# Optimization experiments

Hardware: AMD Instinct MI355X
Metric: run time of the kernel (lower is better)

## Reference

```python
import jax, jax.numpy as jnp
import numpy as np

DECAY_MIN = 0.9
DECAY_MAX = 0.999

def setup_inputs() -> dict:
    key = jax.random.key(0)
    ks = jax.random.split(key, 6)
    B, L, D, M = 8, 4096, 1024, 64
    s = 0.02
    return {
        "x": jax.random.normal(ks[0], (B, L, D), jnp.float32),
        "Wq": jax.random.normal(ks[1], (D, M), jnp.float32) * s,
        "Wk": jax.random.normal(ks[2], (D, M), jnp.float32) * s,
        "Wv": jax.random.normal(ks[3], (D, M), jnp.float32) * s,
        "Wo": jax.random.normal(ks[4], (M, D), jnp.float32) * s,
        "bo": jnp.zeros((D,), jnp.float32),
        "Wg": jax.random.normal(ks[5], (D, 1), jnp.float32) * s,
        "bg": jnp.zeros((1,), jnp.float32),
        "decay_param": jnp.full((1,), 0.5, jnp.float32),
    }

def reference(x, Wq, Wk, Wv, Wo, bo, Wg, bg, decay_param):
    B, L, D = x.shape
    M = Wq.shape[1]
    # decay in [DECAY_MIN, DECAY_MAX], shape (1,) -> scalar broadcast
    decay = DECAY_MIN + jax.nn.sigmoid(decay_param) * (DECAY_MAX - DECAY_MIN)
    q = x @ Wq  # (B,L,M)
    k = x @ Wk
    v = x @ Wv
    gates = jax.nn.sigmoid(x @ Wg + bg)[..., 0]  # (B,L)
    S0 = jnp.zeros((B, M, M), x.dtype)

    def scan_fn(S, inp):
        q_t, k_t, v_t, g_t = inp  # (B,M),(B,M),(B,M),(B,)
        gk = k_t * g_t[:, None]
        gv = v_t * g_t[:, None]
        # fast-weight update: S = decay*S + gk ⊗ gv
        S = decay * S + gk[:, :, None] * gv[:, None, :]
        out_t = jnp.einsum('bd,bde->be', q_t, S)
        return S, out_t

    S_final, outs = jax.lax.scan(
        scan_fn, S0,
        (q.transpose(1, 0, 2), k.transpose(1, 0, 2), v.transpose(1, 0, 2), gates.T))
    outs = outs.transpose(1, 0, 2)  # (B,L,M)
    y = outs @ Wo + bo  # (B,L,D); dropout deterministic (eval)
    return y, S_final
```

## Files before the change

kernel.cpp:

```cpp
#include <hip/hip_runtime.h>
#include <math.h>

#define B_SZ 8
#define L_SZ 4096
#define D_SZ 1024
#define M_SZ 64
#define ROWS (B_SZ * L_SZ)
#define NCHUNK 64
#define CHUNK 64

#define FMA4(acc, sc, v) { (acc).x += (sc)*(v).x; (acc).y += (sc)*(v).y; (acc).z += (sc)*(v).z; (acc).w += (sc)*(v).w; }
#define SCALE4(v, sc) { (v).x *= (sc); (v).y *= (sc); (v).z *= (sc); (v).w *= (sc); }

typedef __attribute__((ext_vector_type(8))) short bf16x8;
typedef __attribute__((ext_vector_type(4))) float f32x4;

__device__ __forceinline__ float sigmoid_f(float z) { return 1.0f / (1.0f + __expf(-z)); }
__device__ __forceinline__ float decay_of(const float* __restrict__ dp) {
  return 0.9f + (0.999f - 0.9f) * sigmoid_f(dp[0]);
}
__device__ __forceinline__ unsigned short f2bf(float f) {
  unsigned int u = __float_as_uint(f);
  unsigned int r = (u + 0x7FFFu + ((u >> 16) & 1u)) >> 16;
  return (unsigned short)r;
}

__global__ __launch_bounds__(256) void k0_prep(
    const float* __restrict__ Wq, const float* __restrict__ Wk,
    const float* __restrict__ Wv, unsigned short* __restrict__ Wt)
{
  const int n = blockIdx.x;
  const float* src = (n < 64) ? Wq : (n < 128) ? Wk : Wv;
  const int nc = n & 63;
  #pragma unroll
  for (int j = 0; j < 4; ++j) {
    int k = threadIdx.x + 256 * j;
    Wt[(size_t)n * D_SZ + k] = f2bf(src[(size_t)k * 64 + nc]);
  }
}

#define K1_ROWS 128
#define K1_LDA 72
#define K1_LDB 72

__global__ __launch_bounds__(256, 1) void k1_qkvg_mfma(
    const float* __restrict__ x, const unsigned short* __restrict__ Wt,
    const float* __restrict__ Wg, const float* __restrict__ bg,
    float* __restrict__ q_ws, float* __restrict__ a_ws, float* __restrict__ b_ws)
{
  __shared__ __align__(16) unsigned short As[K1_ROWS * K1_LDA];
  __shared__ __align__(16) unsigned short Bs[192 * K1_LDB];
  __shared__ float Wgs[64];
  __shared__ float Gs[K1_ROWS];

  const int tid  = threadIdx.x;
  const int lane = tid & 63;
  const int w    = tid >> 6;
  const int quad = lane >> 4;
  const int l15  = lane & 15;
  const int row0 = blockIdx.x * K1_ROWS;

  const int srow = tid >> 1;
  const int skh  = tid & 1;

  f32x4 acc[2][12];
  #pragma unroll
  for (int tr = 0; tr < 2; ++tr)
    #pragma unroll
    for (int tn = 0; tn < 12; ++tn)
      acc[tr][tn] = (f32x4){0.f, 0.f, 0.f, 0.f};

  float gacc = 0.f;

  for (int k0 = 0; k0 < D_SZ; k0 += 64) {
    float4 xa[8];
    const float* xp = x + (size_t)(row0 + srow) * D_SZ + k0 + skh * 32;
    #pragma unroll
    for (int j = 0; j < 8; ++j) xa[j] = *reinterpret_cast<const float4*>(xp + 4 * j);
    uint4 bb[6];
    #pragma unroll
    for (int i = 0; i < 6; ++i) {
      int cid = tid + 256 * i;
      int n = cid >> 3, c = cid & 7;
      bb[i] = *reinterpret_cast<const uint4*>(Wt + (size_t)n * D_SZ + k0 + 8 * c);
    }
    float4 wgv = make_float4(0, 0, 0, 0);
    if (tid < 16) wgv = *reinterpret_cast<const float4*>(Wg + k0 + 4 * tid);

    __syncthreads();

    #pragma unroll
    for (int j = 0; j < 4; ++j) {
      uint4 p;
      p.x = (unsigned)f2bf(xa[2*j].x)   | ((unsigned)f2bf(xa[2*j].y)   << 16);
      p.y = (unsigned)f2bf(xa[2*j].z)   | ((unsigned)f2bf(xa[2*j].w)   << 16);
      p.z = (unsigned)f2bf(xa[2*j+1].x) | ((unsigned)f2bf(xa[2*j+1].y) << 16);
      p.w = (unsigned)f2bf(xa[2*j+1].z) | ((unsigned)f2bf(xa[2*j+1].w) << 16);
      *reinterpret_cast<uint4*>(&As[srow * K1_LDA + skh * 32 + 8 * j]) = p;
    }
    #pragma unroll
    for (int i = 0; i < 6; ++i) {
      int cid = tid + 256 * i;
      int n = cid >> 3, c = cid & 7;
      *reinterpret_cast<uint4*>(&Bs[n * K1_LDB + 8 * c]) = bb[i];
    }
    if (tid < 16) *reinterpret_cast<float4*>(&Wgs[4 * tid]) = wgv;
    __syncthreads();

    #pragma unroll
    for (int j = 0; j < 8; ++j) {
      float4 wv = *reinterpret_cast<float4*>(&Wgs[skh * 32 + 4 * j]);
      gacc += xa[j].x * wv.x + xa[j].y * wv.y + xa[j].z * wv.z + xa[j].w * wv.w;
    }

    #pragma unroll
    for (int kt = 0; kt < 2; ++kt) {
      bf16x8 af0 = *reinterpret_cast<bf16x8*>(&As[(32 * w +      l15) * K1_LDA + kt * 32 + quad * 8]);
      bf16x8 af1 = *reinterpret_cast<bf16x8*>(&As[(32 * w + 16 + l15) * K1_LDA + kt * 32 + quad * 8]);
      #pragma unroll
      for (int tn = 0; tn < 12; ++tn) {
        bf16x8 bfv = *reinterpret_cast<bf16x8*>(&Bs[(tn * 16 + l15) * K1_LDB + kt * 32 + quad * 8]);
        acc[0][tn] = __builtin_amdgcn_mfma_f32_16x16x32_bf16(af0, bfv, acc[0][tn], 0, 0, 0);
        acc[1][tn] = __builtin_amdgcn_mfma_f32_16x16x32_bf16(af1, bfv, acc[1][tn], 0, 0, 0);
      }
    }
  }

  float gfull = gacc + __shfl_xor(gacc, 1);
  if ((tid & 1) == 0) Gs[srow] = sigmoid_f(gfull + bg[0]);
  __syncthreads();

  #pragma unroll
  for (int tr = 0; tr < 2; ++tr) {
    const int rbase = 32 * w + 16 * tr + quad * 4;
    #pragma unroll
    for (int tn = 0; tn < 12; ++tn) {
      const int ncol = (tn & 3) * 16 + l15;
      float* dst = (tn < 4) ? q_ws : (tn < 8 ? a_ws : b_ws);
      #pragma unroll
      for (int r = 0; r < 4; ++r) {
        const int rl = rbase + r;
        float vv = acc[tr][tn][r];
        if (tn >= 4) vv *= Gs[rl];
        dst[(size_t)(row0 + rl) * 64 + ncol] = vv;
      }
    }
  }
}

__global__ __launch_bounds__(256) void k2_delta(
    const float* __restrict__ a_ws, const float* __restrict__ b_ws,
    const float* __restrict__ dp, float* __restrict__ dS)
{
  __shared__ float Aa[64][64];
  __shared__ float Bc[64][64];
  __shared__ float pw[64];
  const int tid = threadIdx.x;
  const int bc = blockIdx.x;
  const int rowbase = (bc >> 6) * L_SZ + (bc & 63) * CHUNK;
  const int s = tid >> 2, m0 = (tid & 3) * 16;
  #pragma unroll
  for (int j = 0; j < 4; ++j) {
    *reinterpret_cast<float4*>(&Aa[s][m0 + 4*j]) =
        *reinterpret_cast<const float4*>(&a_ws[(size_t)(rowbase + s) * 64 + m0 + 4*j]);
    *reinterpret_cast<float4*>(&Bc[s][m0 + 4*j]) =
        *reinterpret_cast<const float4*>(&b_ws[(size_t)(rowbase + s) * 64 + m0 + 4*j]);
  }
  if (tid < 64) pw[tid] = powf(decay_of(dp), (float)(63 - tid));
  __syncthreads();
  const int d0 = tid >> 2, e0 = (tid & 3) * 16;
  float4 o0 = make_float4(0,0,0,0), o1 = o0, o2 = o0, o3 = o0;
  for (int ss = 0; ss < 64; ++ss) {
    float wa = pw[ss] * Aa[ss][d0];
    float4 b0 = *reinterpret_cast<float4*>(&Bc[ss][e0+0]);
    float4 b1 = *reinterpret_cast<float4*>(&Bc[ss][e0+4]);
    float4 b2 = *reinterpret_cast<float4*>(&Bc[ss][e0+8]);
    float4 b3 = *reinterpret_cast<float4*>(&Bc[ss][e0+12]);
    FMA4(o0, wa, b0); FMA4(o1, wa, b1); FMA4(o2, wa, b2); FMA4(o3, wa, b3);
  }
  float* dst = &dS[((size_t)bc << 12) + d0 * 64 + e0];
  *reinterpret_cast<float4*>(dst + 0)  = o0;
  *reinterpret_cast<float4*>(dst + 4)  = o1;
  *reinterpret_cast<float4*>(dst + 8)  = o2;
  *reinterpret_cast<float4*>(dst + 12) = o3;
}

__global__ __launch_bounds__(256) void k3_scan(
    const float* __restrict__ dS, const float* __restrict__ dp,
    float* __restrict__ Sst, float* __restrict__ sfin)
{
  const int g = blockIdx.x * 256 + threadIdx.x;
  const int b = g >> 12;
  const int de = g & 4095;
  const float dC = powf(decay_of(dp), 64.0f);
  float s = 0.f;
  for (int c = 0; c < NCHUNK; ++c) {
    const size_t idx = ((size_t)(b * 64 + c) << 12) + de;
    Sst[idx] = s;
    s = dC * s + dS[idx];
  }
  sfin[((size_t)b << 12) + de] = s;
}

__global__ __launch_bounds__(256) void k4_intra(
    const float* __restrict__ q_ws, const float* __restrict__ a_ws,
    const float* __restrict__ b_ws, const float* __restrict__ Sst,
    const float* __restrict__ dp, float* __restrict__ outs)
{
  __shared__ float Qs[64][68];
  __shared__ float Ps[64][68];
  __shared__ float Bs[64][64];
  __shared__ float S0s[64][64];
  __shared__ float pw[65];
  const int tid = threadIdx.x;
  const int bc = blockIdx.x;
  const int rowbase = (bc >> 6) * L_SZ + (bc & 63) * CHUNK;
  const int s = tid >> 2, m0 = (tid & 3) * 16;
  #pragma unroll
  for (int j = 0; j < 4; ++j) {
    float4 qv = *reinterpret_cast<const float4*>(&q_ws[(size_t)(rowbase + s) * 64 + m0 + 4*j]);
    Qs[s][m0+4*j+0] = qv.x; Qs[s][m0+4*j+1] = qv.y; Qs[s][m0+4*j+2] = qv.z; Qs[s][m0+4*j+3] = qv.w;
    float4 av = *reinterpret_cast<const float4*>(&a_ws[(size_t)(rowbase + s) * 64 + m0 + 4*j]);
    Ps[m0+4*j+0][s] = av.x; Ps[m0+4*j+1][s] = av.y; Ps[m0+4*j+2][s] = av.z; Ps[m0+4*j+3][s] = av.w;
    float4 bv = *reinterpret_cast<const float4*>(&b_ws[(size_t)(rowbase + s) * 64 + m0 + 4*j]);
    *reinterpret_cast<float4*>(&Bs[s][m0+4*j]) = bv;
    float4 sv = *reinterpret_cast<const float4*>(&Sst[((size_t)bc << 12) + tid*16 + 4*j]);
    *reinterpret_cast<float4*>(&(&S0s[0][0])[tid*16 + 4*j]) = sv;
  }
  if (tid < 65) pw[tid] = powf(decay_of(dp), (float)tid);
  __syncthreads();

  const int t0 = tid >> 2, c0 = (tid & 3) * 16;
  float4 r0 = make_float4(0,0,0,0), r1 = r0, r2 = r0, r3 = r0;
  for (int m = 0; m < 64; ++m) {
    float qv = Qs[t0][m];
    float4 a0 = *reinterpret_cast<float4*>(&Ps[m][c0+0]);
    float4 a1 = *reinterpret_cast<float4*>(&Ps[m][c0+4]);
    float4 a2 = *reinterpret_cast<float4*>(&Ps[m][c0+8]);
    float4 a3 = *reinterpret_cast<float4*>(&Ps[m][c0+12]);
    FMA4(r0, qv, a0); FMA4(r1, qv, a1); FMA4(r2, qv, a2); FMA4(r3, qv, a3);
  }
  float rr[16] = {r0.x,r0.y,r0.z,r0.w, r1.x,r1.y,r1.z,r1.w,
                  r2.x,r2.y,r2.z,r2.w, r3.x,r3.y,r3.z,r3.w};
  __syncthreads();
  #pragma unroll
  for (int j = 0; j < 16; ++j) {
    const int sidx = c0 + j;
    Ps[t0][sidx] = (sidx <= t0) ? rr[j] * pw[t0 - sidx] : 0.f;
  }
  __syncthreads();

  float4 o0 = make_float4(0,0,0,0), o1 = o0, o2 = o0, o3 = o0;
  for (int m = 0; m < 64; ++m) {
    float qv = Qs[t0][m];
    float4 v0 = *reinterpret_cast<float4*>(&S0s[m][c0+0]);
    float4 v1 = *reinterpret_cast<float4*>(&S0s[m][c0+4]);
    float4 v2 = *reinterpret_cast<float4*>(&S0s[m][c0+8]);
    float4 v3 = *reinterpret_cast<float4*>(&S0s[m][c0+12]);
    FMA4(o0, qv, v0); FMA4(o1, qv, v1); FMA4(o2, qv, v2); FMA4(o3, qv, v3);
  }
  const float dsc = pw[t0 + 1];
  SCALE4(o0, dsc); SCALE4(o1, dsc); SCALE4(o2, dsc); SCALE4(o3, dsc);
  for (int ss = 0; ss < 64; ++ss) {
    float pv = Ps[t0][ss];
    float4 b0 = *reinterpret_cast<float4*>(&Bs[ss][c0+0]);
    float4 b1 = *reinterpret_cast<float4*>(&Bs[ss][c0+4]);
    float4 b2 = *reinterpret_cast<float4*>(&Bs[ss][c0+8]);
    float4 b3 = *reinterpret_cast<float4*>(&Bs[ss][c0+12]);
    FMA4(o0, pv, b0); FMA4(o1, pv, b1); FMA4(o2, pv, b2); FMA4(o3, pv, b3);
  }
  float* dst = &outs[(size_t)(rowbase + t0) * 64 + c0];
  *reinterpret_cast<float4*>(dst + 0)  = o0;
  *reinterpret_cast<float4*>(dst + 4)  = o1;
  *reinterpret_cast<float4*>(dst + 8)  = o2;
  *reinterpret_cast<float4*>(dst + 12) = o3;
}

__global__ __launch_bounds__(256) void k5_proj(
    const float* __restrict__ outs, const float* __restrict__ Wo,
    const float* __restrict__ bo, float* __restrict__ y)
{
  __shared__ float Os[64][68];
  __shared__ float Ws[64][64];
  const int tid = threadIdx.x;
  const int tx = tid & 15, ty = tid >> 4;
  const int row0 = blockIdx.x * 64;
  const int n0 = blockIdx.y * 64;
  const int s = tid >> 2, m0 = (tid & 3) * 16;
  #pragma unroll
  for (int j = 0; j < 4; ++j) {
    float4 ov = *reinterpret_cast<const float4*>(&outs[(size_t)(row0 + s) * 64 + m0 + 4*j]);
    Os[s][m0+4*j+0] = ov.x; Os[s][m0+4*j+1] = ov.y; Os[s][m0+4*j+2] = ov.z; Os[s][m0+4*j+3] = ov.w;
    float4 wv = *reinterpret_cast<const float4*>(&Wo[(size_t)s * D_SZ + n0 + m0 + 4*j]);
    *reinterpret_cast<float4*>(&Ws[s][m0+4*j]) = wv;
  }
  __syncthreads();
  float4 acc[4];
  #pragma unroll
  for (int r = 0; r < 4; ++r) acc[r] = make_float4(0,0,0,0);
  for (int kk = 0; kk < 64; ++kk) {
    float a0 = Os[4*ty+0][kk];
    float a1 = Os[4*ty+1][kk];
    float a2 = Os[4*ty+2][kk];
    float a3 = Os[4*ty+3][kk];
    float4 w = *reinterpret_cast<float4*>(&Ws[kk][4*tx]);
    FMA4(acc[0], a0, w); FMA4(acc[1], a1, w); FMA4(acc[2], a2, w); FMA4(acc[3], a3, w);
  }
  float4 bv = *reinterpret_cast<const float4*>(&bo[n0 + 4*tx]);
  #pragma unroll
  for (int r = 0; r < 4; ++r) {
    float4 res;
    res.x = acc[r].x + bv.x; res.y = acc[r].y + bv.y;
    res.z = acc[r].z + bv.z; res.w = acc[r].w + bv.w;
    *reinterpret_cast<float4*>(&y[(size_t)(row0 + 4*ty + r) * D_SZ + n0 + 4*tx]) = res;
  }
}

extern "C" void kernel_launch(void* const* d_in, const int* in_sizes, int n_in,
                              void* d_out, int out_size, void* d_ws, size_t ws_size,
                              hipStream_t stream) {
  (void)in_sizes; (void)n_in; (void)out_size; (void)ws_size;
  const float* x  = (const float*)d_in[0];
  const float* Wq = (const float*)d_in[1];
  const float* Wk = (const float*)d_in[2];
  const float* Wv = (const float*)d_in[3];
  const float* Wo = (const float*)d_in[4];
  const float* bo = (const float*)d_in[5];
  const float* Wg = (const float*)d_in[6];
  const float* bg = (const float*)d_in[7];
  const float* dp = (const float*)d_in[8];

  float* y    = (float*)d_out;
  float* sfin = y + (size_t)B_SZ * L_SZ * D_SZ;

  float* ws   = (float*)d_ws;
  const size_t SEG = (size_t)ROWS * M_SZ;
  float* q_ws = ws;
  float* a_ws = q_ws + SEG;
  float* b_ws = a_ws + SEG;
  float* dS   = b_ws + SEG;
  float* Sst  = dS   + SEG;
  float* outs = Sst  + SEG;
  unsigned short* Wt = (unsigned short*)outs;

  k0_prep<<<dim3(192), dim3(256), 0, stream>>>(Wq, Wk, Wv, Wt);
  k1_qkvg_mfma<<<dim3(ROWS / K1_ROWS), dim3(256), 0, stream>>>(x, Wt, Wg, bg, q_ws, a_ws, b_ws);
  k2_delta<<<dim3(B_SZ * NCHUNK), dim3(256), 0, stream>>>(a_ws, b_ws, dp, dS);
  k3_scan<<<dim3((B_SZ * M_SZ * M_SZ) / 256), dim3(256), 0, stream>>>(dS, dp, Sst, sfin);
  k4_intra<<<dim3(B_SZ * NCHUNK), dim3(256), 0, stream>>>(q_ws, a_ws, b_ws, Sst, dp, outs);
  k5_proj<<<dim3(ROWS / 64, D_SZ / 64), dim3(256), 0, stream>>>(outs, Wo, bo, y);
}
```

Measured before the change: 385.6 us.

## Double-buffer QKV GEMM with direct register A-fragments, smaller tiles; batch scan loads

The projection kernel now uses 64-row tiles at two blocks per CU. Each wave loads its x rows from global memory straight into MFMA A-fragments in registers, skipping the LDS staging for A. The weight tile is double-buffered in LDS with the next tile's loads issued before the current MFMAs, so one barrier per iteration remains. The gate is reduced by lane shuffles instead of shared memory. The chunk scan kernel also loads all 64 chunk deltas into registers up front to expose memory-level parallelism. The costs are higher register pressure and B tiles that are now re-read from L2 by twice as many blocks.

```diff
diff --git a/kernel.cpp b/kernel.cpp
--- a/kernel.cpp
+++ b/kernel.cpp
@@ -39,19 +39,16 @@
   }
 }
 
-#define K1_ROWS 128
-#define K1_LDA 72
+#define K1_ROWS 64
 #define K1_LDB 72
 
-__global__ __launch_bounds__(256, 1) void k1_qkvg_mfma(
+__global__ __launch_bounds__(256, 2) void k1_qkvg_mfma(
     const float* __restrict__ x, const unsigned short* __restrict__ Wt,
     const float* __restrict__ Wg, const float* __restrict__ bg,
     float* __restrict__ q_ws, float* __restrict__ a_ws, float* __restrict__ b_ws)
 {
-  __shared__ __align__(16) unsigned short As[K1_ROWS * K1_LDA];
-  __shared__ __align__(16) unsigned short Bs[192 * K1_LDB];
-  __shared__ float Wgs[64];
-  __shared__ float Gs[K1_ROWS];
+  __shared__ __align__(16) unsigned short Bs[2][192 * K1_LDB];
+  __shared__ float Wgs[D_SZ];
 
   const int tid  = threadIdx.x;
   const int lane = tid & 63;
@@ -60,90 +57,101 @@
   const int l15  = lane & 15;
   const int row0 = blockIdx.x * K1_ROWS;
 
-  const int srow = tid >> 1;
-  const int skh  = tid & 1;
-
-  f32x4 acc[2][12];
-  #pragma unroll
-  for (int tr = 0; tr < 2; ++tr)
-    #pragma unroll
-    for (int tn = 0; tn < 12; ++tn)
-      acc[tr][tn] = (f32x4){0.f, 0.f, 0.f, 0.f};
-
-  float gacc = 0.f;
-
-  for (int k0 = 0; k0 < D_SZ; k0 += 64) {
-    float4 xa[8];
-    const float* xp = x + (size_t)(row0 + srow) * D_SZ + k0 + skh * 32;
-    #pragma unroll
-    for (int j = 0; j < 8; ++j) xa[j] = *reinterpret_cast<const float4*>(xp + 4 * j);
-    uint4 bb[6];
+  const float* xrow = x + (size_t)(row0 + 16 * w + l15) * D_SZ;
+
+  f32x4 acc[12];
+  #pragma unroll
+  for (int tn = 0; tn < 12; ++tn) acc[tn] = (f32x4){0.f, 0.f, 0.f, 0.f};
+
+  uint4  bb[6];
+  float4 xa[4];
+  bf16x8 af[2];
+  float  gacc = 0.f;
+
+  *reinterpret_cast<float4*>(&Wgs[4 * tid]) = *reinterpret_cast<const float4*>(Wg + 4 * tid);
+
+  auto loadB = [&](int k0) {
     #pragma unroll
     for (int i = 0; i < 6; ++i) {
       int cid = tid + 256 * i;
       int n = cid >> 3, c = cid & 7;
       bb[i] = *reinterpret_cast<const uint4*>(Wt + (size_t)n * D_SZ + k0 + 8 * c);
     }
-    float4 wgv = make_float4(0, 0, 0, 0);
-    if (tid < 16) wgv = *reinterpret_cast<const float4*>(Wg + k0 + 4 * tid);
-
-    __syncthreads();
-
-    #pragma unroll
-    for (int j = 0; j < 4; ++j) {
-      uint4 p;
-      p.x = (unsigned)f2bf(xa[2*j].x)   | ((unsigned)f2bf(xa[2*j].y)   << 16);
-      p.y = (unsigned)f2bf(xa[2*j].z)   | ((unsigned)f2bf(xa[2*j].w)   << 16);
-      p.z = (unsigned)f2bf(xa[2*j+1].x) | ((unsigned)f2bf(xa[2*j+1].y) << 16);
-      p.w = (unsigned)f2bf(xa[2*j+1].z) | ((unsigned)f2bf(xa[2*j+1].w) << 16);
-      *reinterpret_cast<uint4*>(&As[srow * K1_LDA + skh * 32 + 8 * j]) = p;
-    }
+  };
+  auto loadA = [&](int k0) {
+    #pragma unroll
+    for (int kt = 0; kt < 2; ++kt)
+      #pragma unroll
+      for (int j = 0; j < 2; ++j)
+        xa[kt * 2 + j] = *reinterpret_cast<const float4*>(xrow + k0 + kt * 32 + quad * 8 + 4 * j);
+  };
+  auto writeB = [&](int buf) {
     #pragma unroll
     for (int i = 0; i < 6; ++i) {
       int cid = tid + 256 * i;
       int n = cid >> 3, c = cid & 7;
-      *reinterpret_cast<uint4*>(&Bs[n * K1_LDB + 8 * c]) = bb[i];
-    }
-    if (tid < 16) *reinterpret_cast<float4*>(&Wgs[4 * tid]) = wgv;
-    __syncthreads();
-
-    #pragma unroll
-    for (int j = 0; j < 8; ++j) {
-      float4 wv = *reinterpret_cast<float4*>(&Wgs[skh * 32 + 4 * j]);
-      gacc += xa[j].x * wv.x + xa[j].y * wv.y + xa[j].z * wv.z + xa[j].w * wv.w;
-    }
-
+      *reinterpret_cast<uint4*>(&Bs[buf][n * K1_LDB + 8 * c]) = bb[i];
+    }
+  };
+  auto cvtA = [&](int k0) {
     #pragma unroll
     for (int kt = 0; kt < 2; ++kt) {
-      bf16x8 af0 = *reinterpret_cast<bf16x8*>(&As[(32 * w +      l15) * K1_LDA + kt * 32 + quad * 8]);
-      bf16x8 af1 = *reinterpret_cast<bf16x8*>(&As[(32 * w + 16 + l15) * K1_LDA + kt * 32 + quad * 8]);
-      #pragma unroll
-      for (int tn = 0; tn < 12; ++tn) {
-        bf16x8 bfv = *reinterpret_cast<bf16x8*>(&Bs[(tn * 16 + l15) * K1_LDB + kt * 32 + quad * 8]);
-        acc[0][tn] = __builtin_amdgcn_mfma_f32_16x16x32_bf16(af0, bfv, acc[0][tn], 0, 0, 0);
-        acc[1][tn] = __builtin_amdgcn_mfma_f32_16x16x32_bf16(af1, bfv, acc[1][tn], 0, 0, 0);
-      }
-    }
-  }
-
-  float gfull = gacc + __shfl_xor(gacc, 1);
-  if ((tid & 1) == 0) Gs[srow] = sigmoid_f(gfull + bg[0]);
-  __syncthreads();
-
-  #pragma unroll
-  for (int tr = 0; tr < 2; ++tr) {
-    const int rbase = 32 * w + 16 * tr + quad * 4;
+      float4 lo = xa[kt * 2], hi = xa[kt * 2 + 1];
+      const float* wp = &Wgs[k0 + kt * 32 + quad * 8];
+      float4 w0 = *reinterpret_cast<const float4*>(wp);
+      float4 w1 = *reinterpret_cast<const float4*>(wp + 4);
+      gacc += lo.x * w0.x + lo.y * w0.y + lo.z * w0.z + lo.w * w0.w
+            + hi.x * w1.x + hi.y * w1.y + hi.z * w1.z + hi.w * w1.w;
+      uint4 p;
+      p.x = (unsigned)f2bf(lo.x) | ((unsigned)f2bf(lo.y) << 16);
+      p.y = (unsigned)f2bf(lo.z) | ((unsigned)f2bf(lo.w) << 16);
+      p.z = (unsigned)f2bf(hi.x) | ((unsigned)f2bf(hi.y) << 16);
+      p.w = (unsigned)f2bf(hi.z) | ((unsigned)f2bf(hi.w) << 16);
+      af[kt] = *reinterpret_cast<bf16x8*>(&p);
+    }
+  };
+
+  loadA(0); loadB(0);
+  __syncthreads();
+  writeB(0);
+  cvtA(0);
+  __syncthreads();
+
+  for (int t = 0; t < 16; ++t) {
+    const int cur = t & 1;
+    if (t < 15) { loadA((t + 1) * 64); loadB((t + 1) * 64); }
     #pragma unroll
     for (int tn = 0; tn < 12; ++tn) {
-      const int ncol = (tn & 3) * 16 + l15;
-      float* dst = (tn < 4) ? q_ws : (tn < 8 ? a_ws : b_ws);
-      #pragma unroll
-      for (int r = 0; r < 4; ++r) {
-        const int rl = rbase + r;
-        float vv = acc[tr][tn][r];
-        if (tn >= 4) vv *= Gs[rl];
-        dst[(size_t)(row0 + rl) * 64 + ncol] = vv;
-      }
+      bf16x8 b0 = *reinterpret_cast<bf16x8*>(&Bs[cur][(tn * 16 + l15) * K1_LDB + quad * 8]);
+      bf16x8 b1 = *reinterpret_cast<bf16x8*>(&Bs[cur][(tn * 16 + l15) * K1_LDB + 32 + quad * 8]);
+      acc[tn] = __builtin_amdgcn_mfma_f32_16x16x32_bf16(af[0], b0, acc[tn], 0, 0, 0);
+      acc[tn] = __builtin_amdgcn_mfma_f32_16x16x32_bf16(af[1], b1, acc[tn], 0, 0, 0);
+    }
+    if (t < 15) {
+      writeB(cur ^ 1);
+      cvtA((t + 1) * 64);
+      __syncthreads();
+    }
+  }
+
+  float g = gacc;
+  g += __shfl_xor(g, 16);
+  g += __shfl_xor(g, 32);
+  const float gs = sigmoid_f(g + bg[0]);
+  float gr[4];
+  #pragma unroll
+  for (int r = 0; r < 4; ++r) gr[r] = __shfl(gs, quad * 4 + r);
+
+  #pragma unroll
+  for (int tn = 0; tn < 12; ++tn) {
+    const int ncol = (tn & 3) * 16 + l15;
+    float* dst = (tn < 4) ? q_ws : (tn < 8 ? a_ws : b_ws);
+    #pragma unroll
+    for (int r = 0; r < 4; ++r) {
+      const int rl = 16 * w + quad * 4 + r;
+      float vv = acc[tn][r];
+      if (tn >= 4) vv *= gr[r];
+      dst[(size_t)(row0 + rl) * 64 + ncol] = vv;
     }
   }
 }
@@ -193,11 +201,15 @@
   const int b = g >> 12;
   const int de = g & 4095;
   const float dC = powf(decay_of(dp), 64.0f);
+  const size_t base = ((size_t)(b * 64) << 12) + de;
+  float d[NCHUNK];
+  #pragma unroll
+  for (int c = 0; c < NCHUNK; ++c) d[c] = dS[base + ((size_t)c << 12)];
   float s = 0.f;
+  #pragma unroll
   for (int c = 0; c < NCHUNK; ++c) {
-    const size_t idx = ((size_t)(b * 64 + c) << 12) + de;
-    Sst[idx] = s;
-    s = dC * s + dS[idx];
+    Sst[base + ((size_t)c << 12)] = s;
+    s = dC * s + d[c];
   }
   sfin[((size_t)b << 12) + de] = s;
 }
```

Result: faster. 374.6 us (-2.9%).
